# Kernel optimization log

Hardware: AMD Instinct MI355X
Metric: run time of the kernel (lower is better)

The kernel has to match this reference:

```python
import jax, jax.numpy as jnp
import numpy as np

N = 100000      # nodes (single node type)
E = 400000      # edges per relation
R = 4           # relations
DIN = 128       # h_dim
H1 = 8          # heads, layer 1
DH1 = DIN // H1 # per-head dim, layer 1
DOUT = 128      # out_dim (layer 2 has 1 head of dim DOUT)
NEG_SLOPE = 0.2 # GATConv default leaky_relu slope


def gat_rel_layer(h, src, dst, W, al, ar, loop_w, bias, activation):
    """One RelationalAttLayer: per-relation GATConv (bias=False), summed across
    relations, + self-loop matmul + bias + optional relu. dropout=0.
    h: [N, din]; src/dst: [R, E]; W: [R, din, H*Dh]; al/ar: [R, H, Dh];
    loop_w: [din, dout]; bias: [dout]."""
    n = h.shape[0]

    def per_rel(src_r, dst_r, W_r, al_r, ar_r):
        nh, dh = al_r.shape
        Wh = (h @ W_r).reshape(n, nh, dh)                 # [N,H,Dh]
        el = jnp.sum(Wh * al_r, axis=-1)                  # [N,H]
        er = jnp.sum(Wh * ar_r, axis=-1)                  # [N,H]
        e = jax.nn.leaky_relu(el[src_r] + er[dst_r], NEG_SLOPE)  # [E,H]
        # edge-softmax over incoming edges per destination node (stable)
        m = jax.lax.stop_gradient(jax.ops.segment_max(e, dst_r, num_segments=n))
        ex = jnp.exp(e - m[dst_r])
        denom = jax.ops.segment_sum(ex, dst_r, num_segments=n)  # [N,H]
        alpha = ex / denom[dst_r]                                # [E,H]
        # scatter-aggregate messages
        return jax.ops.segment_sum(alpha[:, :, None] * Wh[src_r], dst_r,
                                   num_segments=n)               # [N,H,Dh]

    outs = jax.vmap(per_rel)(src, dst, W, al, ar)  # [R,N,H,Dh]
    hout = outs.sum(0).reshape(n, -1)              # cross-relation sum, flatten heads
    hout = hout + h @ loop_w + bias                # self-loop + h_bias
    if activation:
        hout = jax.nn.relu(hout)
    return hout


def setup_inputs() -> dict:
    key = jax.random.key(0)
    ks = jax.random.split(key, 14)
    s = 0.1
    return {
        "h": jax.random.normal(ks[0], (N, DIN), dtype=jnp.float32),
        "src_idx": jax.random.randint(ks[1], (R, E), 0, N, dtype=jnp.int32),
        "dst_idx": jax.random.randint(ks[2], (R, E), 0, N, dtype=jnp.int32),
        # layer 1 params (h_dim -> h_dim, H1 heads)
        "W1": jax.random.normal(ks[3], (R, DIN, H1 * DH1), dtype=jnp.float32) * s,
        "al1": jax.random.normal(ks[4], (R, H1, DH1), dtype=jnp.float32) * s,
        "ar1": jax.random.normal(ks[5], (R, H1, DH1), dtype=jnp.float32) * s,
        "loop1": jax.random.normal(ks[6], (DIN, DIN), dtype=jnp.float32) * s,
        "b1": jnp.zeros((DIN,), dtype=jnp.float32),
        # layer 2 params (h_dim -> out_dim, 1 head)
        "W2": jax.random.normal(ks[7], (R, DIN, DOUT), dtype=jnp.float32) * s,
        "al2": jax.random.normal(ks[8], (R, 1, DOUT), dtype=jnp.float32) * s,
        "ar2": jax.random.normal(ks[9], (R, 1, DOUT), dtype=jnp.float32) * s,
        "loop2": jax.random.normal(ks[10], (DIN, DOUT), dtype=jnp.float32) * s,
        "b2": jnp.zeros((DOUT,), dtype=jnp.float32),
    }


def reference(h, src_idx, dst_idx, W1, al1, ar1, loop1, b1,
              W2, al2, ar2, loop2, b2):
    # hidden layer: relu activation; last layer: no activation (last_layer_act=False)
    h1 = gat_rel_layer(h, src_idx, dst_idx, W1, al1, ar1, loop1, b1, activation=True)
    h2 = gat_rel_layer(h1, src_idx, dst_idx, W2, al2, ar2, loop2, b2, activation=False)
    return h2
```

## Files before the change

### kernel.cpp

```cpp
#include <hip/hip_runtime.h>

#define NN 100000
#define NE 400000
#define NREL 4
#define MAXDEG 24

typedef unsigned short u16;
typedef __attribute__((ext_vector_type(8))) short bf16x8;
typedef __attribute__((ext_vector_type(4))) float f32x4;

__device__ __forceinline__ u16 f2bf(float x) {
    union { float f; unsigned int u; } v; v.f = x;
    unsigned int r = v.u + 0x7fffu + ((v.u >> 16) & 1u);
    return (u16)(r >> 16);
}
__device__ __forceinline__ float bf2f(u16 x) {
    union { unsigned int u; float f; } v; v.u = ((unsigned int)x) << 16;
    return v.f;
}

__global__ __launch_bounds__(256) void zero_cnt_kernel(int* __restrict__ cnt, int n)
{
    int i = blockIdx.x * 256 + threadIdx.x;
    if (i < n) cnt[i] = 0;
}

__global__ __launch_bounds__(256) void conv_kernel(
    const float* __restrict__ X, u16* __restrict__ Xb, int n8)
{
    int i = blockIdx.x * 256 + threadIdx.x;
    if (i >= n8) return;
    float4 a = ((const float4*)X)[2 * i];
    float4 b = ((const float4*)X)[2 * i + 1];
    ushort4 lo, hi;
    lo.x = f2bf(a.x); lo.y = f2bf(a.y); lo.z = f2bf(a.z); lo.w = f2bf(a.w);
    hi.x = f2bf(b.x); hi.y = f2bf(b.y); hi.z = f2bf(b.z); hi.w = f2bf(b.w);
    ((ushort4*)Xb)[2 * i] = lo;
    ((ushort4*)Xb)[2 * i + 1] = hi;
}

__global__ __launch_bounds__(256) void build_bcat_kernel(
    const float* __restrict__ W, const float* __restrict__ loopw,
    u16* __restrict__ Bcat)
{
    int id = blockIdx.x * 256 + threadIdx.x;
    if (id >= 5 * 16384) return;
    int slot = id >> 14, rem = id & 16383;
    int c = rem >> 7, k = rem & 127;
    const float* M = (slot < 4) ? (W + slot * 16384) : loopw;
    Bcat[(size_t)c * 640 + slot * 128 + k] = f2bf(M[k * 128 + c]);
}

__global__ __launch_bounds__(256) void build_w_kernel(
    const float* __restrict__ W, const float* __restrict__ al,
    const float* __restrict__ ar, u16* __restrict__ wcatB, int nh, int dh)
{
    int id = blockIdx.x * 256 + threadIdx.x;
    if (id >= 16384) return;
    int j = id >> 7, k = id & 127;
    int P2 = 8 * nh;
    float s = 0.f;
    if (j < P2) {
        int half = 4 * nh;
        int jj = (j < half) ? j : j - half;
        const float* av = (j < half) ? al : ar;
        int r = jj / nh, hh = jj % nh;
        for (int i = 0; i < dh; ++i)
            s += W[r * 16384 + k * 128 + hh * dh + i] * av[(r * nh + hh) * dh + i];
    }
    wcatB[j * 128 + k] = f2bf(s);
}

__global__ __launch_bounds__(256) void csr_build_kernel(
    const int* __restrict__ src, const int* __restrict__ dst,
    int* __restrict__ cur, int* __restrict__ bucket)
{
    int i = blockIdx.x * 256 + threadIdx.x;
    if (i >= NE) return;
    int d0 = dst[i],          s0 = src[i];
    int d1 = dst[NE + i],     s1 = src[NE + i];
    int d2 = dst[2 * NE + i], s2 = src[2 * NE + i];
    int d3 = dst[3 * NE + i], s3 = src[3 * NE + i];
    int p0 = atomicAdd(&cur[d0], 1);
    int p1 = atomicAdd(&cur[NN + d1], 1);
    int p2 = atomicAdd(&cur[2 * NN + d2], 1);
    int p3 = atomicAdd(&cur[3 * NN + d3], 1);
    if (p0 < MAXDEG) bucket[(size_t)d0 * MAXDEG + p0] = s0;
    if (p1 < MAXDEG) bucket[((size_t)NN + d1) * MAXDEG + p1] = s1;
    if (p2 < MAXDEG) bucket[((size_t)2 * NN + d2) * MAXDEG + p2] = s2;
    if (p3 < MAXDEG) bucket[((size_t)3 * NN + d3) * MAXDEG + p3] = s3;
}

__global__ __launch_bounds__(256) void fused_gemm_kernel(
    const u16* __restrict__ Xb, const u16* __restrict__ Bcat,
    const u16* __restrict__ wcatB, u16* __restrict__ Wh,
    float* __restrict__ O, const float* __restrict__ bias,
    float* __restrict__ elrR, int n)
{
    __shared__ u16 sA[128][136];
    __shared__ u16 sB[128][136];
    const int tid = threadIdx.x;
    const int y = blockIdx.y;
    const int row0 = blockIdx.x * 128;
    const u16* bbase; int bstride;
    if (y < 5) { bbase = Bcat + y * 128; bstride = 640; }
    else       { bbase = wcatB;          bstride = 128; }

#pragma unroll
    for (int i = 0; i < 8; ++i) {
        int idx = tid + 256 * i;
        int r = idx >> 4, ch = idx & 15;
        *(float4*)&sB[r][ch * 8] = *(const float4*)(bbase + (size_t)r * bstride + ch * 8);
    }
#pragma unroll
    for (int i = 0; i < 8; ++i) {
        int idx = tid + 256 * i;
        int r = idx >> 4, ch = idx & 15;
        int gr = row0 + r;
        float4 v = make_float4(0.f, 0.f, 0.f, 0.f);
        if (gr < n) v = *(const float4*)(Xb + (size_t)gr * 128 + ch * 8);
        *(float4*)&sA[r][ch * 8] = v;
    }
    __syncthreads();

    const int w = tid >> 6, lane = tid & 63;
    const int lr = lane & 15, hi = lane >> 4;
    f32x4 acc[2][8];
#pragma unroll
    for (int rf = 0; rf < 2; ++rf)
#pragma unroll
        for (int fn = 0; fn < 8; ++fn) acc[rf][fn] = (f32x4){0.f, 0.f, 0.f, 0.f};

#pragma unroll
    for (int ko = 0; ko < 4; ++ko) {
        const int kk = ko * 32 + hi * 8;
        bf16x8 a0 = *(const bf16x8*)&sA[w * 32 + lr][kk];
        bf16x8 a1 = *(const bf16x8*)&sA[w * 32 + 16 + lr][kk];
#pragma unroll
        for (int fn = 0; fn < 8; ++fn) {
            bf16x8 b = *(const bf16x8*)&sB[fn * 16 + lr][kk];
            acc[0][fn] = __builtin_amdgcn_mfma_f32_16x16x32_bf16(a0, b, acc[0][fn], 0, 0, 0);
            acc[1][fn] = __builtin_amdgcn_mfma_f32_16x16x32_bf16(a1, b, acc[1][fn], 0, 0, 0);
        }
    }

    if (y < 4) {
        u16* Wr = Wh + (size_t)y * NN * 128;
#pragma unroll
        for (int rf = 0; rf < 2; ++rf)
#pragma unroll
        for (int reg = 0; reg < 4; ++reg) {
            int grow = row0 + w * 32 + rf * 16 + hi * 4 + reg;
            if (grow >= n) continue;
            u16* crow = Wr + (size_t)grow * 128;
#pragma unroll
            for (int fn = 0; fn < 8; ++fn)
                crow[fn * 16 + lr] = f2bf(acc[rf][fn][reg]);
        }
    } else if (y == 4) {
#pragma unroll
        for (int rf = 0; rf < 2; ++rf)
#pragma unroll
        for (int reg = 0; reg < 4; ++reg) {
            int grow = row0 + w * 32 + rf * 16 + hi * 4 + reg;
            if (grow >= n) continue;
            float* crow = O + (size_t)grow * 128;
#pragma unroll
            for (int fn = 0; fn < 8; ++fn) {
                int col = fn * 16 + lr;
                crow[col] = acc[rf][fn][reg] + bias[col];
            }
        }
    } else {
#pragma unroll
        for (int rf = 0; rf < 2; ++rf)
#pragma unroll
        for (int reg = 0; reg < 4; ++reg) {
            int grow = row0 + w * 32 + rf * 16 + hi * 4 + reg;
            if (grow >= n) continue;
#pragma unroll
            for (int fn = 0; fn < 8; ++fn) {
                int col = fn * 16 + lr;
                if (col < 64) {
                    int jj  = (col < 32) ? col : col - 32;
                    int r   = jj >> 3, hh = jj & 7;
                    int off = (col < 32) ? hh : 8 + hh;
                    elrR[((size_t)r * NN + grow) * 16 + off] = acc[rf][fn][reg];
                }
            }
        }
    }
}

__global__ __launch_bounds__(256) void elr2_gemm_kernel(
    const u16* __restrict__ Xb, const u16* __restrict__ wcatB,
    float* __restrict__ elrR, int n)
{
    __shared__ u16 sA[64][136];
    __shared__ u16 sB[16][136];
    const int tid = threadIdx.x;
    const int row0 = blockIdx.x * 64;

    if (tid < 256) {
        int r = tid >> 4, ch = tid & 15;
        *(float4*)&sB[r][ch * 8] = *(const float4*)(wcatB + (size_t)r * 128 + ch * 8);
    }
#pragma unroll
    for (int i = 0; i < 4; ++i) {
        int idx = tid + 256 * i;
        int r = idx >> 4, ch = idx & 15;
        int gr = row0 + r;
        float4 v = make_float4(0.f, 0.f, 0.f, 0.f);
        if (gr < n) v = *(const float4*)(Xb + (size_t)gr * 128 + ch * 8);
        *(float4*)&sA[r][ch * 8] = v;
    }
    __syncthreads();

    const int w = tid >> 6, lane = tid & 63;
    const int lr = lane & 15, hi = lane >> 4;
    f32x4 acc = (f32x4){0.f, 0.f, 0.f, 0.f};
#pragma unroll
    for (int ko = 0; ko < 4; ++ko) {
        const int kk = ko * 32 + hi * 8;
        bf16x8 a = *(const bf16x8*)&sA[w * 16 + lr][kk];
        bf16x8 b = *(const bf16x8*)&sB[lr][kk];
        acc = __builtin_amdgcn_mfma_f32_16x16x32_bf16(a, b, acc, 0, 0, 0);
    }
#pragma unroll
    for (int reg = 0; reg < 4; ++reg) {
        int grow = row0 + w * 16 + hi * 4 + reg;
        if (grow >= n) continue;
        int col = lr;
        if (col < 8) {
            int r = (col < 4) ? col : col - 4;
            int off = (col < 4) ? 0 : 1;
            elrR[((size_t)r * NN + grow) * 2 + off] = acc[reg];
        }
    }
}

__global__ __launch_bounds__(256) void gather_l1_kernel(
    const int* __restrict__ cnt, const int* __restrict__ bucket,
    const float* __restrict__ elrR, const u16* __restrict__ Wh,
    const float* __restrict__ Oloop, u16* __restrict__ Xb)
{
    const int d = blockIdx.x;
    const int w = threadIdx.x >> 6;
    const int lane = threadIdx.x & 63;
    const int c0 = lane * 2;
    const int hh = c0 >> 4;
    __shared__ float2 part[4][64];

    int deg = cnt[w * NN + d];
    deg = deg < 0 ? 0 : (deg > MAXDEG ? MAXDEG : deg);
    const int* bk = bucket + ((size_t)w * NN + d) * MAXDEG;
    const float* elP = elrR + (size_t)w * NN * 16;
    const float erd = elP[(size_t)d * 16 + 8 + hh];
    const u16* whr = Wh + (size_t)w * NN * 128;

    float dn = 0.f, m0 = 0.f, m1 = 0.f;
    if (deg > 0) {
        int4 q0 = *(const int4*)bk;
        const int ss0[4] = {q0.x, q0.y, q0.z, q0.w};
#pragma unroll
        for (int e = 0; e < 4; ++e) {
            int s = ss0[e];
            s = ((unsigned)s < (unsigned)NN) ? s : 0;
            float v = elP[(size_t)s * 16 + hh] + erd;
            ushort2 wv = *(const ushort2*)(whr + (size_t)s * 128 + c0);
            v = v > 0.f ? v : 0.2f * v;
            float ex = (e < deg) ? __expf(v) : 0.f;
            dn += ex;
            m0 = fmaf(ex, bf2f(wv.x), m0);
            m1 = fmaf(ex, bf2f(wv.y), m1);
        }
        if (deg > 4) {
            int4 q1 = *(const int4*)(bk + 4);
            const int ss1[4] = {q1.x, q1.y, q1.z, q1.w};
#pragma unroll
            for (int e = 0; e < 4; ++e) {
                int s = ss1[e];
                s = ((unsigned)s < (unsigned)NN) ? s : 0;
                float v = elP[(size_t)s * 16 + hh] + erd;
                ushort2 wv = *(const ushort2*)(whr + (size_t)s * 128 + c0);
                v = v > 0.f ? v : 0.2f * v;
                float ex = (e + 4 < deg) ? __expf(v) : 0.f;
                dn += ex;
                m0 = fmaf(ex, bf2f(wv.x), m0);
                m1 = fmaf(ex, bf2f(wv.y), m1);
            }
            for (int e = 8; e < deg; ++e) {
                int s = bk[e];
                s = ((unsigned)s < (unsigned)NN) ? s : 0;
                float v = elP[(size_t)s * 16 + hh] + erd;
                v = v > 0.f ? v : 0.2f * v;
                float ex = __expf(v);
                ushort2 wv = *(const ushort2*)(whr + (size_t)s * 128 + c0);
                dn += ex;
                m0 = fmaf(ex, bf2f(wv.x), m0);
                m1 = fmaf(ex, bf2f(wv.y), m1);
            }
        }
    }
    float inv = (deg > 0) ? 1.f / dn : 0.f;
    part[w][lane] = make_float2(m0 * inv, m1 * inv);
    __syncthreads();
    if (w == 0) {
        float2 a = part[0][lane], b = part[1][lane];
        float2 c = part[2][lane], e4 = part[3][lane];
        float2 ov = *((const float2*)(Oloop + (size_t)d * 128) + lane);
        float r0 = fmaxf(ov.x + a.x + b.x + c.x + e4.x, 0.f);
        float r1 = fmaxf(ov.y + a.y + b.y + c.y + e4.y, 0.f);
        ushort2 o;
        o.x = f2bf(r0); o.y = f2bf(r1);
        *(ushort2*)(Xb + (size_t)d * 128 + c0) = o;
    }
}

__global__ __launch_bounds__(256) void gather_x_kernel(
    const int* __restrict__ cnt, const int* __restrict__ bucket,
    const float* __restrict__ elrR, const u16* __restrict__ Xb,
    u16* __restrict__ Xagg)
{
    const int d = blockIdx.x;
    const int w = threadIdx.x >> 6;
    const int lane = threadIdx.x & 63;
    const int c0 = lane * 2;

    int deg = cnt[w * NN + d];
    deg = deg < 0 ? 0 : (deg > MAXDEG ? MAXDEG : deg);
    const int* bk = bucket + ((size_t)w * NN + d) * MAXDEG;
    const float* elP = elrR + (size_t)w * NN * 2;
    const float erd = elP[(size_t)d * 2 + 1];

    float dn = 0.f, m0 = 0.f, m1 = 0.f;
    if (deg > 0) {
        int4 q0 = *(const int4*)bk;
        const int ss0[4] = {q0.x, q0.y, q0.z, q0.w};
#pragma unroll
        for (int e = 0; e < 4; ++e) {
            int s = ss0[e];
            s = ((unsigned)s < (unsigned)NN) ? s : 0;
            float v = elP[(size_t)s * 2] + erd;
            ushort2 wv = *(const ushort2*)(Xb + (size_t)s * 128 + c0);
            v = v > 0.f ? v : 0.2f * v;
            float ex = (e < deg) ? __expf(v) : 0.f;
            dn += ex;
            m0 = fmaf(ex, bf2f(wv.x), m0);
            m1 = fmaf(ex, bf2f(wv.y), m1);
        }
        if (deg > 4) {
            int4 q1 = *(const int4*)(bk + 4);
            const int ss1[4] = {q1.x, q1.y, q1.z, q1.w};
#pragma unroll
            for (int e = 0; e < 4; ++e) {
                int s = ss1[e];
                s = ((unsigned)s < (unsigned)NN) ? s : 0;
                float v = elP[(size_t)s * 2] + erd;
                ushort2 wv = *(const ushort2*)(Xb + (size_t)s * 128 + c0);
                v = v > 0.f ? v : 0.2f * v;
                float ex = (e + 4 < deg) ? __expf(v) : 0.f;
                dn += ex;
                m0 = fmaf(ex, bf2f(wv.x), m0);
                m1 = fmaf(ex, bf2f(wv.y), m1);
            }
            for (int e = 8; e < deg; ++e) {
                int s = bk[e];
                s = ((unsigned)s < (unsigned)NN) ? s : 0;
                float v = elP[(size_t)s * 2] + erd;
                v = v > 0.f ? v : 0.2f * v;
                float ex = __expf(v);
                ushort2 wv = *(const ushort2*)(Xb + (size_t)s * 128 + c0);
                dn += ex;
                m0 = fmaf(ex, bf2f(wv.x), m0);
                m1 = fmaf(ex, bf2f(wv.y), m1);
            }
        }
    }
    float inv = (deg > 0) ? 1.f / dn : 0.f;
    u16* orow = Xagg + ((size_t)w * NN + d) * 128;
    ushort2 o;
    o.x = f2bf(m0 * inv);
    o.y = f2bf(m1 * inv);
    *(ushort2*)(orow + c0) = o;
}

__global__ __launch_bounds__(256) void big_gemm_kernel(
    const u16* __restrict__ Xagg, const u16* __restrict__ Xb,
    const u16* __restrict__ Bcat, const float* __restrict__ bias,
    float* __restrict__ out, int n)
{
    __shared__ u16 sA[128][136];
    __shared__ u16 sB[128][136];
    const int tid = threadIdx.x;
    const int row0 = blockIdx.x * 128;
    const int w = tid >> 6, lane = tid & 63;
    const int lr = lane & 15, hi = lane >> 4;

    f32x4 acc[2][8];
#pragma unroll
    for (int rf = 0; rf < 2; ++rf)
#pragma unroll
        for (int fn = 0; fn < 8; ++fn) acc[rf][fn] = (f32x4){0.f, 0.f, 0.f, 0.f};

    for (int kc = 0; kc < 5; ++kc) {
        const u16* Amat = (kc < 4) ? (Xagg + (size_t)kc * NN * 128) : Xb;
        if (kc) __syncthreads();
#pragma unroll
        for (int i = 0; i < 8; ++i) {
            int idx = tid + 256 * i;
            int r = idx >> 4, ch = idx & 15;
            *(float4*)&sB[r][ch * 8] =
                *(const float4*)(Bcat + (size_t)r * 640 + kc * 128 + ch * 8);
        }
#pragma unroll
        for (int i = 0; i < 8; ++i) {
            int idx = tid + 256 * i;
            int r = idx >> 4, ch = idx & 15;
            int gr = row0 + r;
            float4 v = make_float4(0.f, 0.f, 0.f, 0.f);
            if (gr < n) v = *(const float4*)(Amat + (size_t)gr * 128 + ch * 8);
            *(float4*)&sA[r][ch * 8] = v;
        }
        __syncthreads();
#pragma unroll
        for (int ko = 0; ko < 4; ++ko) {
            const int kk = ko * 32 + hi * 8;
            bf16x8 a0 = *(const bf16x8*)&sA[w * 32 + lr][kk];
            bf16x8 a1 = *(const bf16x8*)&sA[w * 32 + 16 + lr][kk];
#pragma unroll
            for (int fn = 0; fn < 8; ++fn) {
                bf16x8 b = *(const bf16x8*)&sB[fn * 16 + lr][kk];
                acc[0][fn] = __builtin_amdgcn_mfma_f32_16x16x32_bf16(a0, b, acc[0][fn], 0, 0, 0);
                acc[1][fn] = __builtin_amdgcn_mfma_f32_16x16x32_bf16(a1, b, acc[1][fn], 0, 0, 0);
            }
        }
    }

#pragma unroll
    for (int rf = 0; rf < 2; ++rf)
#pragma unroll
    for (int reg = 0; reg < 4; ++reg) {
        int grow = row0 + w * 32 + rf * 16 + hi * 4 + reg;
        if (grow >= n) continue;
        float* crow = out + (size_t)grow * 128;
#pragma unroll
        for (int fn = 0; fn < 8; ++fn) {
            int col = fn * 16 + lr;
            crow[col] = acc[rf][fn][reg] + bias[col];
        }
    }
}

extern "C" void kernel_launch(void* const* d_in, const int* in_sizes, int n_in,
                              void* d_out, int out_size, void* d_ws, size_t ws_size,
                              hipStream_t stream)
{
    const float* h   = (const float*)d_in[0];
    const int*   src = (const int*)d_in[1];
    const int*   dst = (const int*)d_in[2];
    const float* W1  = (const float*)d_in[3];
    const float* al1 = (const float*)d_in[4];
    const float* ar1 = (const float*)d_in[5];
    const float* lp1 = (const float*)d_in[6];
    const float* b1  = (const float*)d_in[7];
    const float* W2  = (const float*)d_in[8];
    const float* al2 = (const float*)d_in[9];
    const float* ar2 = (const float*)d_in[10];
    const float* lp2 = (const float*)d_in[11];
    const float* b2  = (const float*)d_in[12];

    float* out = (float*)d_out;
    char*  p   = (char*)d_ws;

    const size_t szXb   = (size_t)NN * 128 * 2;
    const size_t szO    = (size_t)NN * 128 * 4;
    const size_t szElr  = (size_t)NREL * NN * 16 * 4;
    const size_t szCnt  = (size_t)NREL * NN * 4;
    const size_t szBkt  = (size_t)NREL * NN * MAXDEG * 4;
    const size_t szBcat = 5 * 16384 * 2;
    const size_t szWc   = 16384 * 2;

    u16*   Xb     = (u16*)p;    p += szXb;
    float* O1     = (float*)p;  p += szO;
    float* elrR   = (float*)p;  p += szElr;
    int*   cnt    = (int*)p;    p += szCnt;
    int*   bucket = (int*)p;    p += szBkt;
    u16*   Bcat   = (u16*)p;    p += szBcat;
    u16*   wcatB  = (u16*)p;    p += szWc;
    u16*   Wh     = (u16*)p;

    const int gg128 = (NN + 127) / 128;
    const int gg64  = (NN + 63) / 64;
    const int n8 = NN * 128 / 8;

    zero_cnt_kernel<<<(NREL * NN + 255) / 256, 256, 0, stream>>>(cnt, NREL * NN);
    csr_build_kernel<<<(NE + 255) / 256, 256, 0, stream>>>(src, dst, cnt, bucket);
    conv_kernel<<<(n8 + 255) / 256, 256, 0, stream>>>(h, Xb, n8);

    build_bcat_kernel<<<(5 * 16384) / 256, 256, 0, stream>>>(W1, lp1, Bcat);
    build_w_kernel<<<16384 / 256, 256, 0, stream>>>(W1, al1, ar1, wcatB, 8, 16);
    fused_gemm_kernel<<<dim3(gg128, 6), 256, 0, stream>>>(
        Xb, Bcat, wcatB, Wh, O1, b1, elrR, NN);
    gather_l1_kernel<<<NN, 256, 0, stream>>>(cnt, bucket, elrR, Wh, O1, Xb);

    build_bcat_kernel<<<(5 * 16384) / 256, 256, 0, stream>>>(W2, lp2, Bcat);
    build_w_kernel<<<16384 / 256, 256, 0, stream>>>(W2, al2, ar2, wcatB, 1, 128);
    elr2_gemm_kernel<<<gg64, 256, 0, stream>>>(Xb, wcatB, elrR, NN);
    gather_x_kernel<<<NN, 256, 0, stream>>>(cnt, bucket, elrR, Xb, Wh);
    big_gemm_kernel<<<gg128, 256, 0, stream>>>(Wh, Xb, Bcat, b2, out, NN);
}
```

Before: 747.9 us.

## Loop six GEMM outputs per block, store self-loop in bf16, split el/er arrays

The fused GEMM now runs all six weight panels inside one block, so the A tile is loaded once and reused instead of being reloaded across six grid rows. The self-loop output is stored as bf16 rather than fp32, which halves its write and read traffic in the gather. The attention logits are split into separate compact el and er arrays (8 floats per node) so the gather reads el with a tighter stride. The trade-offs are less grid parallelism (about 782 blocks instead of roughly 4.7k), extra precision loss on the self-loop term, and workspace aliasing between Xagg and the layer-1 buffers.

```diff
diff --git a/kernel.cpp b/kernel.cpp
--- a/kernel.cpp
+++ b/kernel.cpp
@@ -94,24 +94,16 @@
 __global__ __launch_bounds__(256) void fused_gemm_kernel(
     const u16* __restrict__ Xb, const u16* __restrict__ Bcat,
     const u16* __restrict__ wcatB, u16* __restrict__ Wh,
-    float* __restrict__ O, const float* __restrict__ bias,
-    float* __restrict__ elrR, int n)
+    u16* __restrict__ Obf, const float* __restrict__ bias,
+    float* __restrict__ elL, float* __restrict__ elR, int n)
 {
     __shared__ u16 sA[128][136];
     __shared__ u16 sB[128][136];
     const int tid = threadIdx.x;
-    const int y = blockIdx.y;
     const int row0 = blockIdx.x * 128;
-    const u16* bbase; int bstride;
-    if (y < 5) { bbase = Bcat + y * 128; bstride = 640; }
-    else       { bbase = wcatB;          bstride = 128; }
-
-#pragma unroll
-    for (int i = 0; i < 8; ++i) {
-        int idx = tid + 256 * i;
-        int r = idx >> 4, ch = idx & 15;
-        *(float4*)&sB[r][ch * 8] = *(const float4*)(bbase + (size_t)r * bstride + ch * 8);
-    }
+    const int w = tid >> 6, lane = tid & 63;
+    const int lr = lane & 15, hi = lane >> 4;
+
 #pragma unroll
     for (int i = 0; i < 8; ++i) {
         int idx = tid + 256 * i;
@@ -121,74 +113,85 @@
         if (gr < n) v = *(const float4*)(Xb + (size_t)gr * 128 + ch * 8);
         *(float4*)&sA[r][ch * 8] = v;
     }
-    __syncthreads();
-
-    const int w = tid >> 6, lane = tid & 63;
-    const int lr = lane & 15, hi = lane >> 4;
-    f32x4 acc[2][8];
-#pragma unroll
-    for (int rf = 0; rf < 2; ++rf)
-#pragma unroll
-        for (int fn = 0; fn < 8; ++fn) acc[rf][fn] = (f32x4){0.f, 0.f, 0.f, 0.f};
-
-#pragma unroll
-    for (int ko = 0; ko < 4; ++ko) {
-        const int kk = ko * 32 + hi * 8;
-        bf16x8 a0 = *(const bf16x8*)&sA[w * 32 + lr][kk];
-        bf16x8 a1 = *(const bf16x8*)&sA[w * 32 + 16 + lr][kk];
-#pragma unroll
-        for (int fn = 0; fn < 8; ++fn) {
-            bf16x8 b = *(const bf16x8*)&sB[fn * 16 + lr][kk];
-            acc[0][fn] = __builtin_amdgcn_mfma_f32_16x16x32_bf16(a0, b, acc[0][fn], 0, 0, 0);
-            acc[1][fn] = __builtin_amdgcn_mfma_f32_16x16x32_bf16(a1, b, acc[1][fn], 0, 0, 0);
-        }
-    }
-
-    if (y < 4) {
-        u16* Wr = Wh + (size_t)y * NN * 128;
+
+    for (int j = 0; j < 6; ++j) {
+        const u16* bbase; int bstride;
+        if (j < 5) { bbase = Bcat + j * 128; bstride = 640; }
+        else       { bbase = wcatB;          bstride = 128; }
+#pragma unroll
+        for (int i = 0; i < 8; ++i) {
+            int idx = tid + 256 * i;
+            int r = idx >> 4, ch = idx & 15;
+            *(float4*)&sB[r][ch * 8] =
+                *(const float4*)(bbase + (size_t)r * bstride + ch * 8);
+        }
+        __syncthreads();
+
+        f32x4 acc[2][8];
 #pragma unroll
         for (int rf = 0; rf < 2; ++rf)
 #pragma unroll
-        for (int reg = 0; reg < 4; ++reg) {
-            int grow = row0 + w * 32 + rf * 16 + hi * 4 + reg;
-            if (grow >= n) continue;
-            u16* crow = Wr + (size_t)grow * 128;
-#pragma unroll
-            for (int fn = 0; fn < 8; ++fn)
-                crow[fn * 16 + lr] = f2bf(acc[rf][fn][reg]);
-        }
-    } else if (y == 4) {
-#pragma unroll
-        for (int rf = 0; rf < 2; ++rf)
-#pragma unroll
-        for (int reg = 0; reg < 4; ++reg) {
-            int grow = row0 + w * 32 + rf * 16 + hi * 4 + reg;
-            if (grow >= n) continue;
-            float* crow = O + (size_t)grow * 128;
+            for (int fn = 0; fn < 8; ++fn) acc[rf][fn] = (f32x4){0.f, 0.f, 0.f, 0.f};
+#pragma unroll
+        for (int ko = 0; ko < 4; ++ko) {
+            const int kk = ko * 32 + hi * 8;
+            bf16x8 a0 = *(const bf16x8*)&sA[w * 32 + lr][kk];
+            bf16x8 a1 = *(const bf16x8*)&sA[w * 32 + 16 + lr][kk];
 #pragma unroll
             for (int fn = 0; fn < 8; ++fn) {
-                int col = fn * 16 + lr;
-                crow[col] = acc[rf][fn][reg] + bias[col];
-            }
-        }
-    } else {
-#pragma unroll
-        for (int rf = 0; rf < 2; ++rf)
-#pragma unroll
-        for (int reg = 0; reg < 4; ++reg) {
-            int grow = row0 + w * 32 + rf * 16 + hi * 4 + reg;
-            if (grow >= n) continue;
-#pragma unroll
-            for (int fn = 0; fn < 8; ++fn) {
-                int col = fn * 16 + lr;
-                if (col < 64) {
-                    int jj  = (col < 32) ? col : col - 32;
-                    int r   = jj >> 3, hh = jj & 7;
-                    int off = (col < 32) ? hh : 8 + hh;
-                    elrR[((size_t)r * NN + grow) * 16 + off] = acc[rf][fn][reg];
+                bf16x8 b = *(const bf16x8*)&sB[fn * 16 + lr][kk];
+                acc[0][fn] = __builtin_amdgcn_mfma_f32_16x16x32_bf16(a0, b, acc[0][fn], 0, 0, 0);
+                acc[1][fn] = __builtin_amdgcn_mfma_f32_16x16x32_bf16(a1, b, acc[1][fn], 0, 0, 0);
+            }
+        }
+
+        if (j < 4) {
+            u16* Wr = Wh + (size_t)j * NN * 128;
+#pragma unroll
+            for (int rf = 0; rf < 2; ++rf)
+#pragma unroll
+            for (int reg = 0; reg < 4; ++reg) {
+                int grow = row0 + w * 32 + rf * 16 + hi * 4 + reg;
+                if (grow >= n) continue;
+                u16* crow = Wr + (size_t)grow * 128;
+#pragma unroll
+                for (int fn = 0; fn < 8; ++fn)
+                    crow[fn * 16 + lr] = f2bf(acc[rf][fn][reg]);
+            }
+        } else if (j == 4) {
+#pragma unroll
+            for (int rf = 0; rf < 2; ++rf)
+#pragma unroll
+            for (int reg = 0; reg < 4; ++reg) {
+                int grow = row0 + w * 32 + rf * 16 + hi * 4 + reg;
+                if (grow >= n) continue;
+                u16* crow = Obf + (size_t)grow * 128;
+#pragma unroll
+                for (int fn = 0; fn < 8; ++fn) {
+                    int col = fn * 16 + lr;
+                    crow[col] = f2bf(acc[rf][fn][reg] + bias[col]);
                 }
             }
-        }
+        } else {
+#pragma unroll
+            for (int rf = 0; rf < 2; ++rf)
+#pragma unroll
+            for (int reg = 0; reg < 4; ++reg) {
+                int grow = row0 + w * 32 + rf * 16 + hi * 4 + reg;
+                if (grow >= n) continue;
+#pragma unroll
+                for (int fn = 0; fn < 8; ++fn) {
+                    int col = fn * 16 + lr;
+                    if (col < 64) {
+                        int jj = (col < 32) ? col : col - 32;
+                        int r  = jj >> 3, hh = jj & 7;
+                        float* o = (col < 32) ? elL : elR;
+                        o[((size_t)r * NN + grow) * 8 + hh] = acc[rf][fn][reg];
+                    }
+                }
+            }
+        }
+        __syncthreads();
     }
 }
 
@@ -241,8 +244,9 @@
 
 __global__ __launch_bounds__(256) void gather_l1_kernel(
     const int* __restrict__ cnt, const int* __restrict__ bucket,
-    const float* __restrict__ elrR, const u16* __restrict__ Wh,
-    const float* __restrict__ Oloop, u16* __restrict__ Xb)
+    const float* __restrict__ elL, const float* __restrict__ elR,
+    const u16* __restrict__ Wh, const u16* __restrict__ Oloop,
+    u16* __restrict__ Xb)
 {
     const int d = blockIdx.x;
     const int w = threadIdx.x >> 6;
@@ -254,8 +258,8 @@
     int deg = cnt[w * NN + d];
     deg = deg < 0 ? 0 : (deg > MAXDEG ? MAXDEG : deg);
     const int* bk = bucket + ((size_t)w * NN + d) * MAXDEG;
-    const float* elP = elrR + (size_t)w * NN * 16;
-    const float erd = elP[(size_t)d * 16 + 8 + hh];
+    const float* elP = elL + (size_t)w * NN * 8;
+    const float erd = elR[((size_t)w * NN + d) * 8 + hh];
     const u16* whr = Wh + (size_t)w * NN * 128;
 
     float dn = 0.f, m0 = 0.f, m1 = 0.f;
@@ -266,7 +270,7 @@
         for (int e = 0; e < 4; ++e) {
             int s = ss0[e];
             s = ((unsigned)s < (unsigned)NN) ? s : 0;
-            float v = elP[(size_t)s * 16 + hh] + erd;
+            float v = elP[(size_t)s * 8 + hh] + erd;
             ushort2 wv = *(const ushort2*)(whr + (size_t)s * 128 + c0);
             v = v > 0.f ? v : 0.2f * v;
             float ex = (e < deg) ? __expf(v) : 0.f;
@@ -281,7 +285,7 @@
             for (int e = 0; e < 4; ++e) {
                 int s = ss1[e];
                 s = ((unsigned)s < (unsigned)NN) ? s : 0;
-                float v = elP[(size_t)s * 16 + hh] + erd;
+                float v = elP[(size_t)s * 8 + hh] + erd;
                 ushort2 wv = *(const ushort2*)(whr + (size_t)s * 128 + c0);
                 v = v > 0.f ? v : 0.2f * v;
                 float ex = (e + 4 < deg) ? __expf(v) : 0.f;
@@ -292,7 +296,7 @@
             for (int e = 8; e < deg; ++e) {
                 int s = bk[e];
                 s = ((unsigned)s < (unsigned)NN) ? s : 0;
-                float v = elP[(size_t)s * 16 + hh] + erd;
+                float v = elP[(size_t)s * 8 + hh] + erd;
                 v = v > 0.f ? v : 0.2f * v;
                 float ex = __expf(v);
                 ushort2 wv = *(const ushort2*)(whr + (size_t)s * 128 + c0);
@@ -308,9 +312,9 @@
     if (w == 0) {
         float2 a = part[0][lane], b = part[1][lane];
         float2 c = part[2][lane], e4 = part[3][lane];
-        float2 ov = *((const float2*)(Oloop + (size_t)d * 128) + lane);
-        float r0 = fmaxf(ov.x + a.x + b.x + c.x + e4.x, 0.f);
-        float r1 = fmaxf(ov.y + a.y + b.y + c.y + e4.y, 0.f);
+        ushort2 ov = *((const ushort2*)(Oloop + (size_t)d * 128) + lane);
+        float r0 = fmaxf(bf2f(ov.x) + a.x + b.x + c.x + e4.x, 0.f);
+        float r1 = fmaxf(bf2f(ov.y) + a.y + b.y + c.y + e4.y, 0.f);
         ushort2 o;
         o.x = f2bf(r0); o.y = f2bf(r1);
         *(ushort2*)(Xb + (size_t)d * 128 + c0) = o;
@@ -474,21 +478,27 @@
     char*  p   = (char*)d_ws;
 
     const size_t szXb   = (size_t)NN * 128 * 2;
-    const size_t szO    = (size_t)NN * 128 * 4;
-    const size_t szElr  = (size_t)NREL * NN * 16 * 4;
+    const size_t szElr2 = (size_t)NREL * NN * 2 * 4;
     const size_t szCnt  = (size_t)NREL * NN * 4;
     const size_t szBkt  = (size_t)NREL * NN * MAXDEG * 4;
     const size_t szBcat = 5 * 16384 * 2;
     const size_t szWc   = 16384 * 2;
+    const size_t szO    = (size_t)NN * 128 * 2;
+    const size_t szElL  = (size_t)NREL * NN * 8 * 4;
+    const size_t szElR  = (size_t)NREL * NN * 8 * 4;
 
     u16*   Xb     = (u16*)p;    p += szXb;
-    float* O1     = (float*)p;  p += szO;
-    float* elrR   = (float*)p;  p += szElr;
+    float* elr2   = (float*)p;  p += szElr2;
     int*   cnt    = (int*)p;    p += szCnt;
     int*   bucket = (int*)p;    p += szBkt;
     u16*   Bcat   = (u16*)p;    p += szBcat;
     u16*   wcatB  = (u16*)p;    p += szWc;
-    u16*   Wh     = (u16*)p;
+    char*  region = p;
+    u16*   Obf    = (u16*)region;
+    float* elL    = (float*)(region + szO);
+    float* elR    = (float*)(region + szO + szElL);
+    u16*   Wh     = (u16*)(region + szO + szElL + szElR);
+    u16*   Xagg   = (u16*)region;
 
     const int gg128 = (NN + 127) / 128;
     const int gg64  = (NN + 63) / 64;
@@ -500,13 +510,13 @@
 
     build_bcat_kernel<<<(5 * 16384) / 256, 256, 0, stream>>>(W1, lp1, Bcat);
     build_w_kernel<<<16384 / 256, 256, 0, stream>>>(W1, al1, ar1, wcatB, 8, 16);
-    fused_gemm_kernel<<<dim3(gg128, 6), 256, 0, stream>>>(
-        Xb, Bcat, wcatB, Wh, O1, b1, elrR, NN);
-    gather_l1_kernel<<<NN, 256, 0, stream>>>(cnt, bucket, elrR, Wh, O1, Xb);
+    fused_gemm_kernel<<<gg128, 256, 0, stream>>>(
+        Xb, Bcat, wcatB, Wh, Obf, b1, elL, elR, NN);
+    gather_l1_kernel<<<NN, 256, 0, stream>>>(cnt, bucket, elL, elR, Wh, Obf, Xb);
 
     build_bcat_kernel<<<(5 * 16384) / 256, 256, 0, stream>>>(W2, lp2, Bcat);
     build_w_kernel<<<16384 / 256, 256, 0, stream>>>(W2, al2, ar2, wcatB, 1, 128);
-    elr2_gemm_kernel<<<gg64, 256, 0, stream>>>(Xb, wcatB, elrR, NN);
-    gather_x_kernel<<<NN, 256, 0, stream>>>(cnt, bucket, elrR, Xb, Wh);
-    big_gemm_kernel<<<gg128, 256, 0, stream>>>(Wh, Xb, Bcat, b2, out, NN);
-}
+    elr2_gemm_kernel<<<gg64, 256, 0, stream>>>(Xb, wcatB, elr2, NN);
+    gather_x_kernel<<<NN, 256, 0, stream>>>(cnt, bucket, elr2, Xb, Xagg);
+    big_gemm_kernel<<<gg128, 256, 0, stream>>>(Xagg, Xb, Bcat, b2, out, NN);
+}
```

Measured after the change: 757.6 us. No clear change (+1.3%).
